# Performance work log

Measured on AMD Instinct MI355X. Metric: run time of the kernel, lower is better.

Reference implementation:

```python
import jax, jax.numpy as jnp
import numpy as np

B, T, I, H, L, C = 64, 512, 128, 512, 3, 5


def setup_inputs() -> dict:
    key = jax.random.key(0)
    ks = jax.random.split(key, 2 + 4 * L + 2)
    s = 1.0 / np.sqrt(H)  # PyTorch RNN init range
    inp = {"x": jax.random.normal(ks[0], (B, T, I), dtype=jnp.float32)}
    in_dims = [I] + [H] * (L - 1)
    for l in range(L):
        k0, k1, k2, k3 = ks[1 + 4 * l:5 + 4 * l]
        inp[f"W_ih{l}"] = jax.random.uniform(k0, (H, in_dims[l]), jnp.float32, -s, s)
        inp[f"W_hh{l}"] = jax.random.uniform(k1, (H, H), jnp.float32, -s, s)
        inp[f"b_ih{l}"] = jax.random.uniform(k2, (H,), jnp.float32, -s, s)
        inp[f"b_hh{l}"] = jax.random.uniform(k3, (H,), jnp.float32, -s, s)
    so = 1.0 / np.sqrt(H)
    inp["W_out"] = jax.random.uniform(ks[-2], (C, H), jnp.float32, -so, so)
    inp["b_out"] = jax.random.uniform(ks[-1], (C,), jnp.float32, -so, so)
    return inp


def _rnn_layer(xs, W_ih, W_hh, b_ih, b_hh):
    # xs: [B, T, D] -> hidden sequence [B, T, H], ReLU RNN recurrence
    h0 = jnp.zeros((xs.shape[0], W_hh.shape[0]), xs.dtype)
    xproj = jnp.einsum('btd,hd->bth', xs, W_ih) + (b_ih + b_hh)  # precompute input GEMM

    def step(h, xp_t):
        h = jax.nn.relu(xp_t + h @ W_hh.T)
        return h, h

    _, ys = jax.lax.scan(step, h0, jnp.swapaxes(xproj, 0, 1))  # scan over time
    return jnp.swapaxes(ys, 0, 1)


def reference(x, W_ih0, W_hh0, b_ih0, b_hh0, W_ih1, W_hh1, b_ih1, b_hh1,
              W_ih2, W_hh2, b_ih2, b_hh2, W_out, b_out):
    h = x
    for W_ih, W_hh, b_ih, b_hh in ((W_ih0, W_hh0, b_ih0, b_hh0),
                                   (W_ih1, W_hh1, b_ih1, b_hh1),
                                   (W_ih2, W_hh2, b_ih2, b_hh2)):
        h = _rnn_layer(h, W_ih, W_hh, b_ih, b_hh)
    # last timestep -> linear head: [B, C]
    return h[:, -1, :] @ W_out.T + b_out
```

## Files before the change

kernel.cpp:

```cpp
#include <hip/hip_runtime.h>

#define BB 64
#define TT 512
#define II 128
#define HH 512
#define CC 5

__global__ __launch_bounds__(256) void gemm_bias_kernel(
    const float* __restrict__ A, const float* __restrict__ W,
    const float* __restrict__ b1, const float* __restrict__ b2,
    float* __restrict__ out, int K)
{
    __shared__ float As[16][132];
    __shared__ float Bs[16][132];
    const int tid = threadIdx.x;
    const int bm = blockIdx.x;
    const int bn = blockIdx.y;
    const int tx = tid & 15;
    const int ty = tid >> 4;
    const int lr = tid >> 2;
    const int lk = (tid & 3) << 2;

    const float* Ab = A + (size_t)bm * 128 * K;
    const float* Wb = W + (size_t)bn * 128 * K;

    float acc[8][8];
#pragma unroll
    for (int i = 0; i < 8; ++i)
#pragma unroll
        for (int j = 0; j < 8; ++j) acc[i][j] = 0.f;

    for (int k0 = 0; k0 < K; k0 += 16) {
        float4 a0 = *(const float4*)(Ab + (size_t)lr * K + k0 + lk);
        float4 a1 = *(const float4*)(Ab + (size_t)(lr + 64) * K + k0 + lk);
        float4 w0 = *(const float4*)(Wb + (size_t)lr * K + k0 + lk);
        float4 w1 = *(const float4*)(Wb + (size_t)(lr + 64) * K + k0 + lk);
        __syncthreads();
        As[lk + 0][lr] = a0.x; As[lk + 1][lr] = a0.y; As[lk + 2][lr] = a0.z; As[lk + 3][lr] = a0.w;
        As[lk + 0][lr + 64] = a1.x; As[lk + 1][lr + 64] = a1.y; As[lk + 2][lr + 64] = a1.z; As[lk + 3][lr + 64] = a1.w;
        Bs[lk + 0][lr] = w0.x; Bs[lk + 1][lr] = w0.y; Bs[lk + 2][lr] = w0.z; Bs[lk + 3][lr] = w0.w;
        Bs[lk + 0][lr + 64] = w1.x; Bs[lk + 1][lr + 64] = w1.y; Bs[lk + 2][lr + 64] = w1.z; Bs[lk + 3][lr + 64] = w1.w;
        __syncthreads();
#pragma unroll
        for (int k = 0; k < 16; ++k) {
            float4 av0 = *(const float4*)&As[k][ty * 8];
            float4 av1 = *(const float4*)&As[k][ty * 8 + 4];
            float4 bv0 = *(const float4*)&Bs[k][tx * 8];
            float4 bv1 = *(const float4*)&Bs[k][tx * 8 + 4];
            float a[8] = {av0.x, av0.y, av0.z, av0.w, av1.x, av1.y, av1.z, av1.w};
            float b[8] = {bv0.x, bv0.y, bv0.z, bv0.w, bv1.x, bv1.y, bv1.z, bv1.w};
#pragma unroll
            for (int i = 0; i < 8; ++i)
#pragma unroll
                for (int j = 0; j < 8; ++j)
                    acc[i][j] = fmaf(a[i], b[j], acc[i][j]);
        }
    }

    const int nb = bn * 128 + tx * 8;
    float bias[8];
#pragma unroll
    for (int j = 0; j < 8; ++j) bias[j] = b1[nb + j] + b2[nb + j];
#pragma unroll
    for (int i = 0; i < 8; ++i) {
        const size_t m = (size_t)bm * 128 + ty * 8 + i;
        float4 o0 = {acc[i][0] + bias[0], acc[i][1] + bias[1], acc[i][2] + bias[2], acc[i][3] + bias[3]};
        float4 o1 = {acc[i][4] + bias[4], acc[i][5] + bias[5], acc[i][6] + bias[6], acc[i][7] + bias[7]};
        *(float4*)(out + m * HH + nb) = o0;
        *(float4*)(out + m * HH + nb + 4) = o1;
    }
}

__global__ __launch_bounds__(512)
__attribute__((amdgpu_waves_per_eu(2, 2)))
void scan_kernel(
    const float* __restrict__ xp, const float* __restrict__ Whh,
    float* __restrict__ y, unsigned int* hbuf)
{
    __shared__ float hbs[2][2][8 * 68];

    const int tid  = threadIdx.x;
    const int s    = blockIdx.x >> 5;
    const int g    = blockIdx.x & 31;
    const int lane = tid & 63;
    const int wv   = tid >> 6;
    const int rloc = lane >> 3;
    const int kseg = lane & 7;
    const int R    = s * 64 + wv * 8 + rloc;

    const float* wr = Whh + (size_t)R * HH + kseg * 64;
    const float4 w0  = *(const float4*)(wr + 0);
    const float4 w1  = *(const float4*)(wr + 4);
    const float4 w2  = *(const float4*)(wr + 8);
    const float4 w3  = *(const float4*)(wr + 12);
    const float4 w4  = *(const float4*)(wr + 16);
    const float4 w5  = *(const float4*)(wr + 20);
    const float4 w6  = *(const float4*)(wr + 24);
    const float4 w7  = *(const float4*)(wr + 28);
    const float4 w8  = *(const float4*)(wr + 32);
    const float4 w9  = *(const float4*)(wr + 36);
    const float4 w10 = *(const float4*)(wr + 40);
    const float4 w11 = *(const float4*)(wr + 44);
    const float4 w12 = *(const float4*)(wr + 48);
    const float4 w13 = *(const float4*)(wr + 52);
    const float4 w14 = *(const float4*)(wr + 56);
    const float4 w15 = *(const float4*)(wr + 60);

    unsigned int* gbase = hbuf + (size_t)g * 2048;
    const int gb0 = g * 2, gb1 = g * 2 + 1;

    const int lds_w = (tid >> 6) * 68 + (tid & 63);

    hbs[0][0][lds_w] = 0.f;
    hbs[0][1][lds_w] = 0.f;

    const bool pub = (kseg == 0);
    float xp0 = 0.f, xp1 = 0.f;
    if (pub) {
        xp0 = xp[(size_t)gb0 * TT * HH + R];
        xp1 = xp[(size_t)gb1 * TT * HH + R];
    }
    __syncthreads();

    for (int t = 0; t < TT; ++t) {
        const int p = t & 1;

        float a0 = 0.f, a1 = 0.f, c0 = 0.f, c1 = 0.f;
        const float* h0p = &hbs[p][0][kseg * 68];
        const float* h1p = &hbs[p][1][kseg * 68];
#define STEP4(WQ, OFF)                                                   \
        {                                                                \
            float4 h0 = *(const float4*)(h0p + (OFF));                   \
            float4 h1 = *(const float4*)(h1p + (OFF));                   \
            a0 = fmaf(WQ.x, h0.x, a0); a1 = fmaf(WQ.y, h0.y, a1);        \
            a0 = fmaf(WQ.z, h0.z, a0); a1 = fmaf(WQ.w, h0.w, a1);        \
            c0 = fmaf(WQ.x, h1.x, c0); c1 = fmaf(WQ.y, h1.y, c1);        \
            c0 = fmaf(WQ.z, h1.z, c0); c1 = fmaf(WQ.w, h1.w, c1);        \
        }
        STEP4(w0, 0)   STEP4(w1, 4)   STEP4(w2, 8)   STEP4(w3, 12)
        STEP4(w4, 16)  STEP4(w5, 20)  STEP4(w6, 24)  STEP4(w7, 28)
        STEP4(w8, 32)  STEP4(w9, 36)  STEP4(w10, 40) STEP4(w11, 44)
        STEP4(w12, 48) STEP4(w13, 52) STEP4(w14, 56) STEP4(w15, 60)
#undef STEP4

        float A = a0 + a1, Bv = c0 + c1;
        A  += __shfl_xor(A, 1);  A  += __shfl_xor(A, 2);  A  += __shfl_xor(A, 4);
        Bv += __shfl_xor(Bv, 1); Bv += __shfl_xor(Bv, 2); Bv += __shfl_xor(Bv, 4);

        const int q = t + 1;
        unsigned int* slotp = gbase + (q & 1) * 1024;
        const unsigned int phase = (unsigned int)(((q + 1) >> 1) & 1);

        if (pub) {
            const float hn0 = fmaxf(A + xp0, 0.f);
            const float hn1 = fmaxf(Bv + xp1, 0.f);
            if (q < TT) {
                __hip_atomic_store(slotp + R, __float_as_uint(hn0) | (phase << 31),
                                   __ATOMIC_RELAXED, __HIP_MEMORY_SCOPE_AGENT);
                __hip_atomic_store(slotp + 512 + R, __float_as_uint(hn1) | (phase << 31),
                                   __ATOMIC_RELAXED, __HIP_MEMORY_SCOPE_AGENT);
            }
            y[((size_t)gb0 * TT + t) * HH + R] = hn0;
            y[((size_t)gb1 * TT + t) * HH + R] = hn1;
            if (q < TT) {
                xp0 = xp[((size_t)gb0 * TT + q) * HH + R];
                xp1 = xp[((size_t)gb1 * TT + q) * HH + R];
            }
        }

        if (q < TT) {
            unsigned int* s0 = slotp + tid;
            unsigned int* s1 = slotp + 512 + tid;
            unsigned int u0, u1;
            for (;;) {
                u0 = __hip_atomic_load(s0, __ATOMIC_RELAXED, __HIP_MEMORY_SCOPE_AGENT);
                u1 = __hip_atomic_load(s1, __ATOMIC_RELAXED, __HIP_MEMORY_SCOPE_AGENT);
                if (((u0 >> 31) == phase) && ((u1 >> 31) == phase)) break;
            }
            hbs[q & 1][0][lds_w] = __uint_as_float(u0 & 0x7fffffffu);
            hbs[q & 1][1][lds_w] = __uint_as_float(u1 & 0x7fffffffu);
        }
        __syncthreads();
    }
}

__global__ __launch_bounds__(64) void head_kernel(
    const float* __restrict__ y2, const float* __restrict__ Wout,
    const float* __restrict__ bout, float* __restrict__ out)
{
    const int bc = blockIdx.x;
    const int b = bc / CC, c = bc % CC;
    const int lane = threadIdx.x;
    const float* yrow = y2 + ((size_t)b * TT + (TT - 1)) * HH;
    const float* wrow = Wout + (size_t)c * HH;
    float s = 0.f;
#pragma unroll
    for (int i = 0; i < HH / 64; ++i)
        s = fmaf(yrow[lane + 64 * i], wrow[lane + 64 * i], s);
#pragma unroll
    for (int off = 32; off > 0; off >>= 1) s += __shfl_down(s, off);
    if (lane == 0) out[bc] = s + bout[c];
}

extern "C" void kernel_launch(void* const* d_in, const int* in_sizes, int n_in,
                              void* d_out, int out_size, void* d_ws, size_t ws_size,
                              hipStream_t stream)
{
    const float* x = (const float*)d_in[0];
    const float* W_ih[3] = {(const float*)d_in[1], (const float*)d_in[5], (const float*)d_in[9]};
    const float* W_hh[3] = {(const float*)d_in[2], (const float*)d_in[6], (const float*)d_in[10]};
    const float* b_ih[3] = {(const float*)d_in[3], (const float*)d_in[7], (const float*)d_in[11]};
    const float* b_hh[3] = {(const float*)d_in[4], (const float*)d_in[8], (const float*)d_in[12]};
    const float* W_out = (const float*)d_in[13];
    const float* b_out = (const float*)d_in[14];
    float* out = (float*)d_out;

    float* ws   = (float*)d_ws;
    float* Y    = ws;
    float* XP   = ws + (size_t)BB * TT * HH;
    unsigned int* hbuf = (unsigned int*)(XP + (size_t)BB * TT * HH);

    const size_t hbuf_bytes = 32 * 2 * 1024 * sizeof(unsigned int);
    const dim3 ggrid(256, 4, 1);

    gemm_bias_kernel<<<ggrid, 256, 0, stream>>>(x, W_ih[0], b_ih[0], b_hh[0], XP, II);
    hipMemsetAsync(hbuf, 0, hbuf_bytes, stream);
    scan_kernel<<<256, 512, 0, stream>>>(XP, W_hh[0], Y, hbuf);
    gemm_bias_kernel<<<ggrid, 256, 0, stream>>>(Y, W_ih[1], b_ih[1], b_hh[1], XP, HH);
    hipMemsetAsync(hbuf, 0, hbuf_bytes, stream);
    scan_kernel<<<256, 512, 0, stream>>>(XP, W_hh[1], Y, hbuf);
    gemm_bias_kernel<<<ggrid, 256, 0, stream>>>(Y, W_ih[2], b_ih[2], b_hh[2], XP, HH);
    hipMemsetAsync(hbuf, 0, hbuf_bytes, stream);
    scan_kernel<<<256, 512, 0, stream>>>(XP, W_hh[2], Y, hbuf);
    head_kernel<<<BB * CC, 64, 0, stream>>>(Y, W_out, b_out, out);
}
```

Measured before the change: 2.723 ms.

## Pack paired hidden values into 64-bit flags and skip polling own slice

The two batch rows' hidden values are packed into one 64-bit atomic, so each step needs one store and one poll load per element instead of two. The wave whose slice matches the block's own rows writes its results straight to LDS and does not poll global memory. Output stores and xp loads are moved after a sched_barrier so they leave the critical path, and xp is prefetched two steps ahead. This targets per-step cross-block synchronisation latency in the recurrent scan, at the cost of more register state and a reordered memory schedule.

```diff
diff --git a/kernel.cpp b/kernel.cpp
--- a/kernel.cpp
+++ b/kernel.cpp
@@ -75,7 +75,7 @@
 __attribute__((amdgpu_waves_per_eu(2, 2)))
 void scan_kernel(
     const float* __restrict__ xp, const float* __restrict__ Whh,
-    float* __restrict__ y, unsigned int* hbuf)
+    float* __restrict__ y, unsigned long long* hbuf)
 {
     __shared__ float hbs[2][2][8 * 68];
 
@@ -106,19 +106,23 @@
     const float4 w14 = *(const float4*)(wr + 56);
     const float4 w15 = *(const float4*)(wr + 60);
 
-    unsigned int* gbase = hbuf + (size_t)g * 2048;
+    unsigned long long* gbase = hbuf + (size_t)g * 1024;
     const int gb0 = g * 2, gb1 = g * 2 + 1;
 
-    const int lds_w = (tid >> 6) * 68 + (tid & 63);
+    const int lds_w    = wv * 68 + lane;
+    const int self_lds = s * 68 + wv * 8 + rloc;
+    const bool pub     = (kseg == 0);
+    const bool foreign = (wv != s);
 
     hbs[0][0][lds_w] = 0.f;
     hbs[0][1][lds_w] = 0.f;
 
-    const bool pub = (kseg == 0);
-    float xp0 = 0.f, xp1 = 0.f;
+    float xpa0 = 0.f, xpa1 = 0.f, xpb0 = 0.f, xpb1 = 0.f;
     if (pub) {
-        xp0 = xp[(size_t)gb0 * TT * HH + R];
-        xp1 = xp[(size_t)gb1 * TT * HH + R];
+        xpa0 = xp[(size_t)gb0 * TT * HH + R];
+        xpa1 = xp[(size_t)gb1 * TT * HH + R];
+        xpb0 = xp[((size_t)gb0 * TT + 1) * HH + R];
+        xpb1 = xp[((size_t)gb1 * TT + 1) * HH + R];
     }
     __syncthreads();
 
@@ -148,37 +152,45 @@
         Bv += __shfl_xor(Bv, 1); Bv += __shfl_xor(Bv, 2); Bv += __shfl_xor(Bv, 4);
 
         const int q = t + 1;
-        unsigned int* slotp = gbase + (q & 1) * 1024;
+        unsigned long long* slotp = gbase + (q & 1) * 512;
         const unsigned int phase = (unsigned int)(((q + 1) >> 1) & 1);
 
+        float hn0 = 0.f, hn1 = 0.f;
         if (pub) {
-            const float hn0 = fmaxf(A + xp0, 0.f);
-            const float hn1 = fmaxf(Bv + xp1, 0.f);
+            hn0 = fmaxf(A + xpa0, 0.f);
+            hn1 = fmaxf(Bv + xpa1, 0.f);
             if (q < TT) {
-                __hip_atomic_store(slotp + R, __float_as_uint(hn0) | (phase << 31),
-                                   __ATOMIC_RELAXED, __HIP_MEMORY_SCOPE_AGENT);
-                __hip_atomic_store(slotp + 512 + R, __float_as_uint(hn1) | (phase << 31),
+                const unsigned long long pkt =
+                    (unsigned long long)(__float_as_uint(hn0) | (phase << 31)) |
+                    ((unsigned long long)(__float_as_uint(hn1) | (phase << 31)) << 32);
+                __hip_atomic_store(slotp + R, pkt,
                                    __ATOMIC_RELAXED, __HIP_MEMORY_SCOPE_AGENT);
             }
+            hbs[q & 1][0][self_lds] = hn0;
+            hbs[q & 1][1][self_lds] = hn1;
+        }
+
+        if (foreign && q < TT) {
+            unsigned long long u;
+            for (;;) {
+                u = __hip_atomic_load(slotp + tid, __ATOMIC_RELAXED, __HIP_MEMORY_SCOPE_AGENT);
+                if ((((unsigned int)(u >> 31) & 1u) == phase) &&
+                    ((unsigned int)(u >> 63) == phase)) break;
+            }
+            hbs[q & 1][0][lds_w] = __uint_as_float((unsigned int)u & 0x7fffffffu);
+            hbs[q & 1][1][lds_w] = __uint_as_float((unsigned int)(u >> 32) & 0x7fffffffu);
+        }
+
+        __builtin_amdgcn_sched_barrier(0);
+
+        if (pub) {
             y[((size_t)gb0 * TT + t) * HH + R] = hn0;
             y[((size_t)gb1 * TT + t) * HH + R] = hn1;
-            if (q < TT) {
-                xp0 = xp[((size_t)gb0 * TT + q) * HH + R];
-                xp1 = xp[((size_t)gb1 * TT + q) * HH + R];
+            xpa0 = xpb0; xpa1 = xpb1;
+            if (t + 2 < TT) {
+                xpb0 = xp[((size_t)gb0 * TT + t + 2) * HH + R];
+                xpb1 = xp[((size_t)gb1 * TT + t + 2) * HH + R];
             }
-        }
-
-        if (q < TT) {
-            unsigned int* s0 = slotp + tid;
-            unsigned int* s1 = slotp + 512 + tid;
-            unsigned int u0, u1;
-            for (;;) {
-                u0 = __hip_atomic_load(s0, __ATOMIC_RELAXED, __HIP_MEMORY_SCOPE_AGENT);
-                u1 = __hip_atomic_load(s1, __ATOMIC_RELAXED, __HIP_MEMORY_SCOPE_AGENT);
-                if (((u0 >> 31) == phase) && ((u1 >> 31) == phase)) break;
-            }
-            hbs[q & 1][0][lds_w] = __uint_as_float(u0 & 0x7fffffffu);
-            hbs[q & 1][1][lds_w] = __uint_as_float(u1 & 0x7fffffffu);
         }
         __syncthreads();
     }
@@ -218,9 +230,9 @@
     float* ws   = (float*)d_ws;
     float* Y    = ws;
     float* XP   = ws + (size_t)BB * TT * HH;
-    unsigned int* hbuf = (unsigned int*)(XP + (size_t)BB * TT * HH);
-
-    const size_t hbuf_bytes = 32 * 2 * 1024 * sizeof(unsigned int);
+    unsigned long long* hbuf = (unsigned long long*)(XP + (size_t)BB * TT * HH);
+
+    const size_t hbuf_bytes = 32 * 2 * 512 * sizeof(unsigned long long);
     const dim3 ggrid(256, 4, 1);
 
     gemm_bias_kernel<<<ggrid, 256, 0, stream>>>(x, W_ih[0], b_ih[0], b_hh[0], XP, II);
```

Measured after the change: 4.070 ms. 49.5% more time.
